# Kernel tuning notes

Measured on AMD Instinct MI355X. Metric: run time of the kernel, lower is better.

Reference implementation:

```python
import jax, jax.numpy as jnp
import numpy as np

HEADS = 4
KS = 7  # neighborhood window size


def group_norm(x, g, b, eps=1e-5):
    # GroupNorm(1, C) on NCHW: normalize over (C,H,W) per sample
    mu = x.mean(axis=(1, 2, 3), keepdims=True)
    var = x.var(axis=(1, 2, 3), keepdims=True)
    xn = (x - mu) * jax.lax.rsqrt(var + eps)
    return xn * g[None, :, None, None] + b[None, :, None, None]


def layer_norm(x, g, b, eps=1e-5):
    mu = x.mean(axis=-1, keepdims=True)
    var = x.var(axis=-1, keepdims=True)
    return (x - mu) * jax.lax.rsqrt(var + eps) * g + b


def na2d(x, qkv_w, qkv_b, proj_w, proj_b, rpb):
    # Neighborhood attention 2D (NATTEN semantics: window clamped at borders)
    N, H, W, C = x.shape
    e, k = HEADS, KS
    d = C // e
    qkv = x @ qkv_w.T + qkv_b  # [N,H,W,3C]
    q, kk, v = jnp.split(qkv, 3, axis=-1)
    q = q.reshape(N, H, W, e, d) * (d ** -0.5)
    kk = kk.reshape(N, H, W, e, d)
    v = v.reshape(N, H, W, e, d)
    ni = jnp.clip(jnp.arange(H) - k // 2, 0, H - k)[:, None] + jnp.arange(k)  # [H,k]
    nj = jnp.clip(jnp.arange(W) - k // 2, 0, W - k)[:, None] + jnp.arange(k)  # [W,k]
    kg = kk[:, ni][:, :, :, nj]  # [N,H,i,W,j,e,d]
    vg = v[:, ni][:, :, :, nj]
    scores = jnp.einsum('nhwed,nhiwjed->nhweij', q, kg)  # [N,H,W,e,k,k]
    ri = ni - jnp.arange(H)[:, None] + (k - 1)  # rel pos index in [0, 2k-2]
    rj = nj - jnp.arange(W)[:, None] + (k - 1)
    bias = rpb[:, ri][:, :, :, rj]  # [e,H,i,W,j]
    scores = scores + bias.transpose(1, 3, 0, 2, 4)[None]
    attn = jax.nn.softmax(scores.reshape(N, H, W, e, k * k), axis=-1).reshape(N, H, W, e, k, k)
    out = jnp.einsum('nhweij,nhiwjed->nhwed', attn, vg).reshape(N, H, W, C)
    return out @ proj_w.T + proj_b


def na_layer(x, gn_g, gn_b, qkv_w, qkv_b, proj_w, proj_b, rpb, ln_g, ln_b, fc1_w, fc1_b, fc2_w, fc2_b):
    N, C, H, W = x.shape
    x1 = x.transpose(0, 2, 3, 1)  # n h w c (pre-norm residual)
    xg = group_norm(x, gn_g, gn_b).transpose(0, 2, 3, 1)
    a = na2d(xg, qkv_w, qkv_b, proj_w, proj_b, rpb) + x1
    t = a.reshape(N, H * W, C)
    h = jax.nn.gelu(layer_norm(t, ln_g, ln_b) @ fc1_w.T + fc1_b, approximate=False)
    t = t + (h @ fc2_w.T + fc2_b)
    return t.reshape(N, H, W, C).transpose(0, 3, 1, 2)


def conv3x3(x, w, b):
    y = jax.lax.conv_general_dilated(x, w, (1, 1), 'SAME', dimension_numbers=('NCHW', 'OIHW', 'NCHW'))
    return y + b[None, :, None, None]


def setup_inputs() -> dict:
    key = jax.random.key(0)
    ks = jax.random.split(key, 16)
    N, C, H, W = 2, 128, 64, 64
    L, e, k, hid, red = 2, HEADS, KS, 4 * 128, 18
    rn = lambda kk, shape, s=0.02: jax.random.normal(kk, shape, jnp.float32) * s
    return {
        'x': jax.random.normal(ks[0], (N, C, H, W), jnp.float32),
        'gn_g': jnp.ones((L, C), jnp.float32), 'gn_b': jnp.zeros((L, C), jnp.float32),
        'qkv_w': rn(ks[1], (L, 3 * C, C)), 'qkv_b': jnp.zeros((L, 3 * C), jnp.float32),
        'proj_w': rn(ks[2], (L, C, C)), 'proj_b': jnp.zeros((L, C), jnp.float32),
        'rpb': rn(ks[3], (L, e, 2 * k - 1, 2 * k - 1)),
        'ln_g': jnp.ones((L, C), jnp.float32), 'ln_b': jnp.zeros((L, C), jnp.float32),
        'fc1_w': rn(ks[4], (L, hid, C)), 'fc1_b': jnp.zeros((L, hid), jnp.float32),
        'fc2_w': rn(ks[5], (L, C, hid)), 'fc2_b': jnp.zeros((L, C), jnp.float32),
        'bconv_w': rn(ks[6], (C, C, 3, 3)), 'bconv_b': jnp.zeros((C,), jnp.float32),
        'c1_w': rn(ks[7], (C // 4, C)), 'c1_b': jnp.zeros((C // 4,), jnp.float32),
        'c2_w': rn(ks[8], (C, C // 4)), 'c2_b': jnp.zeros((C,), jnp.float32),
        'ca1_w': rn(ks[9], (C // red, C)), 'ca1_b': jnp.zeros((C // red,), jnp.float32),
        'ca2_w': rn(ks[10], (C, C // red)), 'ca2_b': jnp.zeros((C,), jnp.float32),
    }


def reference(x, gn_g, gn_b, qkv_w, qkv_b, proj_w, proj_b, rpb, ln_g, ln_b, fc1_w, fc1_b, fc2_w, fc2_b, bconv_w, bconv_b, c1_w, c1_b, c2_w, c2_b, ca1_w, ca1_b, ca2_w, ca2_b):
    res = x
    for l in range(gn_g.shape[0]):  # n_resblocks (structurally fixed, small)
        res = na_layer(res, gn_g[l], gn_b[l], qkv_w[l], qkv_b[l], proj_w[l], proj_b[l], rpb[l],
                       ln_g[l], ln_b[l], fc1_w[l], fc1_b[l], fc2_w[l], fc2_b[l])
    res = conv3x3(res, bconv_w, bconv_b)
    # tail: 1x1 conv -> ReLU -> 1x1 conv -> CALayer
    y = jax.nn.relu(jnp.einsum('rc,nchw->nrhw', c1_w, res) + c1_b[None, :, None, None])
    y = jnp.einsum('cr,nrhw->nchw', c2_w, y) + c2_b[None, :, None, None]
    p = y.mean(axis=(2, 3))  # global avg pool -> [N,C]
    s = jax.nn.sigmoid(jax.nn.relu(p @ ca1_w.T + ca1_b) @ ca2_w.T + ca2_b)
    y = y * s[:, :, None, None]
    return y + x
```

## Files before the change

### kernel.cpp

```cpp
#include <hip/hip_runtime.h>
#include <math.h>

typedef unsigned short u16;

#define NN 2
#define CC 128
#define HH 64
#define WW 64
#define NHD 4
#define DH 32
#define KSZ 7
#define PIX (NN*HH*WW)
#define HID 512
#define C4 32
#define CRED 7
#define RW 22
#define RNB 160
#define NBV 154

typedef float f32x4 __attribute__((ext_vector_type(4)));
typedef short bf16x8 __attribute__((ext_vector_type(8)));

static __device__ __forceinline__ float u2f(u16 u){ return __uint_as_float(((unsigned)u) << 16); }
static __device__ __forceinline__ u16 f2u(float f){
    unsigned b = __float_as_uint(f);
    return (u16)((b + 0x7FFFu + ((b >> 16) & 1u)) >> 16);
}

__global__ void detect_k(const u16* __restrict__ x, int* __restrict__ flag,
                         float* __restrict__ poolacc){
    __shared__ float red[256];
    int t = threadIdx.x;
    float mx = 0.f;
    for(int i = t; i < 4096; i += 256){
        float v = fabsf(u2f(x[i]));
        if(v < 1e30f) mx = fmaxf(mx, v);
    }
    red[t] = mx; __syncthreads();
    for(int s = 128; s > 0; s >>= 1){
        if(t < s) red[t] = fmaxf(red[t], red[t+s]);
        __syncthreads();
    }
    if(t == 0) *flag = (red[0] > 1e6f) ? 1 : 0;
    if(t < NN*CC) poolacc[t] = 0.f;
}

struct PtrTab { const void* p[23]; int off[24]; };
#define NCVT 2172
#define NRPK 576
#define NNCH 512

__global__ __launch_bounds__(256) void setup_k(
    PtrTab tab, u16* __restrict__ Wb, u16* __restrict__ Wt,
    const void* __restrict__ convw, const void* __restrict__ x,
    float* __restrict__ cur, float* __restrict__ part,
    const int* __restrict__ flag, int total)
{
    int blk = blockIdx.x;
    int t = threadIdx.x;
    int fl = *flag;
    if(blk < NCVT){
        int i = blk*256 + t;
        if(i < total){
            int a = 0;
            while(i >= tab.off[a+1]) a++;
            int loc = i - tab.off[a];
            Wb[i] = fl ? f2u(((const float*)tab.p[a])[loc]) : ((const u16*)tab.p[a])[loc];
        }
        return;
    }
    if(blk < NCVT + NRPK){
        int i = (blk - NCVT)*256 + t;
        if(i < CC*CC*9){
            int o = i/(9*CC); int rem = i%(9*CC); int tap = rem/CC; int c = rem%CC;
            size_t s = (size_t)(o*CC + c)*9 + tap;
            Wt[i] = fl ? f2u(((const float*)convw)[s]) : ((const u16*)convw)[s];
        }
        return;
    }
    __shared__ float tile[32][65];
    __shared__ float wred[4][2];
    int u = blk - NCVT - NRPK;
    int bx = u & 3, by = u >> 2;
    int n = by >> 6, i = by & 63;
    for(int idx = t; idx < 32*64; idx += 256){
        int cl = idx >> 6, j = idx & 63;
        size_t src = ((size_t)(n*CC + bx*32 + cl)*HH + i)*WW + j;
        tile[cl][j] = fl ? ((const float*)x)[src] : u2f(((const u16*)x)[src]);
    }
    __syncthreads();
    float s = 0.f, q = 0.f;
    for(int idx = t; idx < 64*32; idx += 256){
        int j = idx >> 5, cl = idx & 31;
        float v = tile[cl][j];
        cur[((size_t)((n*HH + i)*WW) + j)*CC + bx*32 + cl] = v;
        s += v; q += v*v;
    }
    #pragma unroll
    for(int off = 32; off > 0; off >>= 1){ s += __shfl_xor(s, off, 64); q += __shfl_xor(q, off, 64); }
    int wave = t >> 6;
    if((t & 63) == 0){ wred[wave][0] = s; wred[wave][1] = q; }
    __syncthreads();
    if(t == 0){
        float ss = wred[0][0]+wred[1][0]+wred[2][0]+wred[3][0];
        float qq = wred[0][1]+wred[1][1]+wred[2][1]+wred[3][1];
        int pidx = n*256 + i*4 + bx;
        part[pidx*2] = ss; part[pidx*2+1] = qq;
    }
}

enum { EPI_NONE = 0, EPI_RES = 1, EPI_GELU = 2 };
enum { OUT_F32 = 0, OUT_BF16 = 1, OUT_BOTH = 2 };
enum { EX_NONE = 0, EX_STATS = 1 };
#define LDP 136

template<int EPI, int OUTM, int AGN, int EXTRA>
__global__ __launch_bounds__(256) void g64_k(
    const void* __restrict__ Av, const u16* __restrict__ W, const u16* __restrict__ bias,
    const float* __restrict__ R, float* __restrict__ Cf, u16* __restrict__ Cb,
    const u16* __restrict__ gnw, const u16* __restrict__ gnb,
    float* __restrict__ gnpart, int gncount,
    int M, int N, int K)
{
    __shared__ __align__(16) u16 As[64*LDP];
    __shared__ __align__(16) u16 Bs[64*LDP];
    __shared__ float wred[4][2];
    const int bm = blockIdx.y*64, bn = blockIdx.x*64;
    const int t = threadIdx.x;
    const int wave = t >> 6, lane = t & 63;
    const int wm = (wave >> 1)*32, wn = (wave & 1)*32;
    const int lg = lane >> 4, lr = lane & 15;
    const int nsm = bm >> 12;
    f32x4 acc[2][2];
    #pragma unroll
    for(int i = 0; i < 2; i++)
        #pragma unroll
        for(int j = 0; j < 2; j++) acc[i][j] = (f32x4){0.f,0.f,0.f,0.f};

    float gmu = 0.f, grs = 0.f;
    if(AGN){
        float a = 0.f, q = 0.f;
        for(int idx = lane; idx < gncount; idx += 64){
            a += gnpart[(nsm*gncount + idx)*2];
            q += gnpart[(nsm*gncount + idx)*2 + 1];
        }
        #pragma unroll
        for(int off = 32; off > 0; off >>= 1){
            a += __shfl_xor(a, off, 64); q += __shfl_xor(q, off, 64);
        }
        const float inv = 1.f/(float)(HH*WW*CC);
        gmu = a*inv;
        grs = rsqrtf(fmaxf(q*inv - gmu*gmu, 0.f) + 1e-5f);
    }

    for(int k0 = 0; k0 < K; k0 += 128){
        uint4 ra[4], rb[4];
        float4 fa[4][2];
        #pragma unroll
        for(int r = 0; r < 4; r++){
            int e = r*256 + t;
            int row = e >> 4, ch = e & 15;
            if(AGN){
                const float* ap = (const float*)Av + (size_t)(bm+row)*K + k0 + ch*8;
                fa[r][0] = *(const float4*)ap;
                fa[r][1] = *(const float4*)(ap + 4);
            } else {
                ra[r] = *(const uint4*)((const u16*)Av + (size_t)(bm+row)*K + k0 + ch*8);
            }
            rb[r] = (bn+row < N) ? *(const uint4*)(W + (size_t)(bn+row)*K + k0 + ch*8)
                                 : (uint4){0,0,0,0};
        }
        #pragma unroll
        for(int r = 0; r < 4; r++){
            int e = r*256 + t;
            int row = e >> 4, ch = e & 15;
            if(AGN){
                union { uint4 u; u16 h[8]; } g8, b8, o8;
                g8.u = *(const uint4*)(gnw + k0 + ch*8);
                b8.u = *(const uint4*)(gnb + k0 + ch*8);
                const float* fv = (const float*)&fa[r][0];
                #pragma unroll
                for(int z = 0; z < 8; z++)
                    o8.h[z] = f2u((fv[z]-gmu)*grs*u2f(g8.h[z]) + u2f(b8.h[z]));
                *(uint4*)&As[row*LDP + ch*8] = o8.u;
            } else {
                *(uint4*)&As[row*LDP + ch*8] = ra[r];
            }
            *(uint4*)&Bs[row*LDP + ch*8] = rb[r];
        }
        __syncthreads();
        #pragma unroll
        for(int kc = 0; kc < 4; kc++){
            bf16x8 af0 = *(const bf16x8*)&As[(wm + lr)*LDP      + kc*32 + lg*8];
            bf16x8 af1 = *(const bf16x8*)&As[(wm + 16 + lr)*LDP + kc*32 + lg*8];
            bf16x8 bf0 = *(const bf16x8*)&Bs[(wn + lr)*LDP      + kc*32 + lg*8];
            bf16x8 bf1 = *(const bf16x8*)&Bs[(wn + 16 + lr)*LDP + kc*32 + lg*8];
            acc[0][0] = __builtin_amdgcn_mfma_f32_16x16x32_bf16(af0, bf0, acc[0][0], 0, 0, 0);
            acc[0][1] = __builtin_amdgcn_mfma_f32_16x16x32_bf16(af0, bf1, acc[0][1], 0, 0, 0);
            acc[1][0] = __builtin_amdgcn_mfma_f32_16x16x32_bf16(af1, bf0, acc[1][0], 0, 0, 0);
            acc[1][1] = __builtin_amdgcn_mfma_f32_16x16x32_bf16(af1, bf1, acc[1][1], 0, 0, 0);
        }
        if(k0 + 128 < K) __syncthreads();
    }

    float ssum = 0.f, sq = 0.f;
    #pragma unroll
    for(int i = 0; i < 2; i++){
        #pragma unroll
        for(int j = 0; j < 2; j++){
            int col = bn + wn + j*16 + lr;
            if(col >= N) continue;
            #pragma unroll
            for(int reg = 0; reg < 4; reg++){
                int row = bm + wm + i*16 + lg*4 + reg;
                float v = acc[i][j][reg] + u2f(bias[col]);
                if(EPI == EPI_RES)  v += R[(size_t)row*N + col];
                if(EPI == EPI_GELU) v = 0.5f*v*(1.f + erff(v*0.70710678118f));
                if(OUTM == OUT_F32 || OUTM == OUT_BOTH) Cf[(size_t)row*N + col] = v;
                if(OUTM == OUT_BF16 || OUTM == OUT_BOTH) Cb[(size_t)row*N + col] = f2u(v);
                if(EXTRA == EX_STATS){ ssum += v; sq += v*v; }
            }
        }
    }
    if(EXTRA == EX_STATS){
        #pragma unroll
        for(int off = 32; off > 0; off >>= 1){
            ssum += __shfl_xor(ssum, off, 64); sq += __shfl_xor(sq, off, 64);
        }
        if(lane == 0){ wred[wave][0] = ssum; wred[wave][1] = sq; }
        __syncthreads();
        if(t == 0){
            int bidx = blockIdx.y*gridDim.x + blockIdx.x;
            gnpart[bidx*2]   = wred[0][0]+wred[1][0]+wred[2][0]+wred[3][0];
            gnpart[bidx*2+1] = wred[0][1]+wred[1][1]+wred[2][1]+wred[3][1];
        }
    }
}

__global__ __launch_bounds__(256) void proj_ln_k(
    const u16* __restrict__ A, const u16* __restrict__ W, const u16* __restrict__ bias,
    const float* __restrict__ R, const u16* __restrict__ lng, const u16* __restrict__ lnb,
    float* __restrict__ abuf, u16* __restrict__ lnout)
{
    __shared__ __align__(16) u16 As[64*LDP];
    __shared__ __align__(16) u16 Bs[128*LDP];
    __shared__ float redS[64][2], redQ[64][2], muS[64], rsS[64];
    const int bm = blockIdx.x*64;
    const int t = threadIdx.x;
    const int wave = t >> 6, lane = t & 63;
    const int wm = (wave >> 1)*32, wn = (wave & 1)*64;
    const int lg = lane >> 4, lr = lane & 15;

    {
        uint4 ra[4], rb[8];
        #pragma unroll
        for(int r = 0; r < 4; r++){
            int e = r*256 + t; int row = e >> 4, ch = e & 15;
            ra[r] = *(const uint4*)(A + (size_t)(bm+row)*CC + ch*8);
        }
        #pragma unroll
        for(int r = 0; r < 8; r++){
            int e = r*256 + t; int row = e >> 4, ch = e & 15;
            rb[r] = *(const uint4*)(W + (size_t)row*CC + ch*8);
        }
        #pragma unroll
        for(int r = 0; r < 4; r++){
            int e = r*256 + t; int row = e >> 4, ch = e & 15;
            *(uint4*)&As[row*LDP + ch*8] = ra[r];
        }
        #pragma unroll
        for(int r = 0; r < 8; r++){
            int e = r*256 + t; int row = e >> 4, ch = e & 15;
            *(uint4*)&Bs[row*LDP + ch*8] = rb[r];
        }
    }
    __syncthreads();

    f32x4 acc[2][4];
    #pragma unroll
    for(int i = 0; i < 2; i++)
        #pragma unroll
        for(int j = 0; j < 4; j++) acc[i][j] = (f32x4){0.f,0.f,0.f,0.f};
    #pragma unroll
    for(int kc = 0; kc < 4; kc++){
        bf16x8 af[2], bf[4];
        #pragma unroll
        for(int i = 0; i < 2; i++)
            af[i] = *(const bf16x8*)&As[(wm + i*16 + lr)*LDP + kc*32 + lg*8];
        #pragma unroll
        for(int j = 0; j < 4; j++)
            bf[j] = *(const bf16x8*)&Bs[(wn + j*16 + lr)*LDP + kc*32 + lg*8];
        #pragma unroll
        for(int i = 0; i < 2; i++)
            #pragma unroll
            for(int j = 0; j < 4; j++)
                acc[i][j] = __builtin_amdgcn_mfma_f32_16x16x32_bf16(af[i], bf[j], acc[i][j], 0, 0, 0);
    }
    #pragma unroll
    for(int i = 0; i < 2; i++){
        #pragma unroll
        for(int reg = 0; reg < 4; reg++){
            int rl = wm + i*16 + lg*4 + reg;
            float rs_ = 0.f, rq_ = 0.f;
            #pragma unroll
            for(int j = 0; j < 4; j++){
                int col = wn + j*16 + lr;
                float v = acc[i][j][reg] + u2f(bias[col]) + R[(size_t)(bm+rl)*CC + col];
                acc[i][j][reg] = v;
                abuf[(size_t)(bm+rl)*CC + col] = v;
                rs_ += v; rq_ += v*v;
            }
            rs_ += __shfl_xor(rs_, 1, 64); rq_ += __shfl_xor(rq_, 1, 64);
            rs_ += __shfl_xor(rs_, 2, 64); rq_ += __shfl_xor(rq_, 2, 64);
            rs_ += __shfl_xor(rs_, 4, 64); rq_ += __shfl_xor(rq_, 4, 64);
            rs_ += __shfl_xor(rs_, 8, 64); rq_ += __shfl_xor(rq_, 8, 64);
            if(lr == 0){ redS[rl][wn>>6] = rs_; redQ[rl][wn>>6] = rq_; }
        }
    }
    __syncthreads();
    if(t < 64){
        float mu = (redS[t][0] + redS[t][1])*(1.f/CC);
        float var = fmaxf((redQ[t][0] + redQ[t][1])*(1.f/CC) - mu*mu, 0.f);
        muS[t] = mu; rsS[t] = rsqrtf(var + 1e-5f);
    }
    __syncthreads();
    #pragma unroll
    for(int i = 0; i < 2; i++){
        #pragma unroll
        for(int reg = 0; reg < 4; reg++){
            int rl = wm + i*16 + lg*4 + reg;
            float mu = muS[rl], rstd = rsS[rl];
            #pragma unroll
            for(int j = 0; j < 4; j++){
                int col = wn + j*16 + lr;
                float v = (acc[i][j][reg] - mu)*rstd*u2f(lng[col]) + u2f(lnb[col]);
                lnout[(size_t)(bm+rl)*CC + col] = f2u(v);
            }
        }
    }
}

__global__ __launch_bounds__(256) void mconv_k(
    const u16* __restrict__ in, const u16* __restrict__ Wt,
    const u16* __restrict__ bias, u16* __restrict__ Cb)
{
    __shared__ __align__(16) u16 As[64*LDP];
    __shared__ __align__(16) u16 Bs[64*LDP];
    const int bm = blockIdx.y*64, bn = blockIdx.x*64;
    const int t = threadIdx.x;
    const int wave = t >> 6, lane = t & 63;
    const int wm = (wave >> 1)*32, wn = (wave & 1)*32;
    const int lg = lane >> 4, lr = lane & 15;
    f32x4 acc[2][2];
    #pragma unroll
    for(int i = 0; i < 2; i++)
        #pragma unroll
        for(int j = 0; j < 2; j++) acc[i][j] = (f32x4){0.f,0.f,0.f,0.f};

    for(int tap = 0; tap < 9; tap++){
        int dy = tap/3 - 1, dx = tap%3 - 1;
        int k0 = tap*128;
        uint4 ra[4], rb[4];
        #pragma unroll
        for(int r = 0; r < 4; r++){
            int e = r*256 + t;
            int row = e >> 4, ch = e & 15;
            int p = bm + row;
            int n = p >> 12, ii = (p & 4095) >> 6, jj = p & 63;
            int y = ii + dy, x = jj + dx;
            ra[r] = (uint4){0,0,0,0};
            if(y >= 0 && y < HH && x >= 0 && x < WW)
                ra[r] = *(const uint4*)(in + (size_t)(((n*HH + y)*WW + x))*CC + ch*8);
            rb[r] = *(const uint4*)(Wt + (size_t)(bn+row)*(9*CC) + k0 + ch*8);
        }
        #pragma unroll
        for(int r = 0; r < 4; r++){
            int e = r*256 + t;
            int row = e >> 4, ch = e & 15;
            *(uint4*)&As[row*LDP + ch*8] = ra[r];
            *(uint4*)&Bs[row*LDP + ch*8] = rb[r];
        }
        __syncthreads();
        #pragma unroll
        for(int kc = 0; kc < 4; kc++){
            bf16x8 af0 = *(const bf16x8*)&As[(wm + lr)*LDP      + kc*32 + lg*8];
            bf16x8 af1 = *(const bf16x8*)&As[(wm + 16 + lr)*LDP + kc*32 + lg*8];
            bf16x8 bf0 = *(const bf16x8*)&Bs[(wn + lr)*LDP      + kc*32 + lg*8];
            bf16x8 bf1 = *(const bf16x8*)&Bs[(wn + 16 + lr)*LDP + kc*32 + lg*8];
            acc[0][0] = __builtin_amdgcn_mfma_f32_16x16x32_bf16(af0, bf0, acc[0][0], 0, 0, 0);
            acc[0][1] = __builtin_amdgcn_mfma_f32_16x16x32_bf16(af0, bf1, acc[0][1], 0, 0, 0);
            acc[1][0] = __builtin_amdgcn_mfma_f32_16x16x32_bf16(af1, bf0, acc[1][0], 0, 0, 0);
            acc[1][1] = __builtin_amdgcn_mfma_f32_16x16x32_bf16(af1, bf1, acc[1][1], 0, 0, 0);
        }
        if(tap < 8) __syncthreads();
    }
    #pragma unroll
    for(int i = 0; i < 2; i++){
        #pragma unroll
        for(int j = 0; j < 2; j++){
            int col = bn + wn + j*16 + lr;
            #pragma unroll
            for(int reg = 0; reg < 4; reg++){
                int row = bm + wm + i*16 + lg*4 + reg;
                Cb[(size_t)row*CC + col] = f2u(acc[i][j][reg] + u2f(bias[col]));
            }
        }
    }
}

#define KVP 72
#define PSP 168

__global__ __launch_bounds__(128) void att_tile_k(
    const u16* __restrict__ qkv, const u16* __restrict__ rpb, u16* __restrict__ out)
{
    __shared__ __align__(16) u16 KV[2][RNB][KVP];
    __shared__ __align__(16) u16 Qs[16][64];
    __shared__ __align__(16) u16 Ps[2][16][PSP];
    __shared__ float rpbs[2][169];
    const int blk = blockIdx.x;
    const int rb = blk >> 1, eg = blk & 1;
    const int p0 = rb*16;
    const int jb = p0 & 63, i = (p0 >> 6) & 63, n = p0 >> 12;
    const int i0 = min(max(i-3, 0), HH-KSZ);
    const int rc0 = min(max(jb-3, 0), WW-KSZ);
    const int t = threadIdx.x;

    for(int idx = t; idx < 2*169; idx += 128)
        rpbs[idx/169][idx%169] = u2f(rpb[(eg*2 + idx/169)*169 + idx%169]);
    {
        int pix = t >> 3, ch = t & 7;
        *(uint4*)&Qs[pix][ch*8] = *(const uint4*)(qkv + (size_t)(p0+pix)*(3*CC) + eg*64 + ch*8);
    }
    for(int idx = t; idx < RNB*16; idx += 128){
        int nb = idx >> 4, part = idx & 15;
        int kv = part >> 3, ch = part & 7;
        uint4 v = (uint4){0,0,0,0};
        if(nb < NBV){
            int ky = nb/RW, kcol = nb - ky*RW;
            int sy = i0 + ky, sx = min(rc0 + kcol, WW-1);
            v = *(const uint4*)(qkv + (size_t)((n*HH + sy)*WW + sx)*(3*CC) + CC + kv*CC + eg*64 + ch*8);
        }
        *(uint4*)&KV[kv][nb][ch*8] = v;
    }
    __syncthreads();

    const int el = t >> 6;
    const int lane = t & 63, lg = lane >> 4, lr = lane & 15;

    bf16x8 aq = *(const bf16x8*)&Qs[lr][el*32 + lg*8];
    f32x4 sc[10];
    #pragma unroll
    for(int c = 0; c < 10; c++){
        bf16x8 bk = *(const bf16x8*)&KV[0][c*16+lr][el*32 + lg*8];
        sc[c] = __builtin_amdgcn_mfma_f32_16x16x32_bf16(aq, bk, (f32x4){0.f,0.f,0.f,0.f}, 0, 0, 0);
    }
    #pragma unroll
    for(int reg = 0; reg < 4; reg++){
        int pix = lg*4 + reg;
        int j = jb + pix;
        int base = min(max(j-3, 0), WW-KSZ) - rc0;
        float mx = -1e30f;
        #pragma unroll
        for(int c = 0; c < 10; c++){
            int nb = c*16 + lr;
            int ky = nb/RW, kcol = nb - ky*RW;
            float v = -1e30f;
            if(nb < NBV && kcol >= base && kcol <= base+6){
                int ri = i0 + ky - i + (KSZ-1);
                int rj = rc0 + kcol - j + (KSZ-1);
                v = sc[c][reg]*0.17677669529663689f + rpbs[el][ri*13 + rj];
            }
            sc[c][reg] = v;
            mx = fmaxf(mx, v);
        }
        mx = fmaxf(mx, __shfl_xor(mx, 1, 64));
        mx = fmaxf(mx, __shfl_xor(mx, 2, 64));
        mx = fmaxf(mx, __shfl_xor(mx, 4, 64));
        mx = fmaxf(mx, __shfl_xor(mx, 8, 64));
        float sum = 0.f;
        #pragma unroll
        for(int c = 0; c < 10; c++){
            float p = __expf(sc[c][reg] - mx);
            sc[c][reg] = p; sum += p;
        }
        sum += __shfl_xor(sum, 1, 64);
        sum += __shfl_xor(sum, 2, 64);
        sum += __shfl_xor(sum, 4, 64);
        sum += __shfl_xor(sum, 8, 64);
        float rs = 1.f/sum;
        #pragma unroll
        for(int c = 0; c < 10; c++)
            Ps[el][pix][c*16+lr] = f2u(sc[c][reg]*rs);
    }
    __syncthreads();
    f32x4 o0 = (f32x4){0.f,0.f,0.f,0.f}, o1 = (f32x4){0.f,0.f,0.f,0.f};
    #pragma unroll
    for(int ks = 0; ks < 5; ks++){
        bf16x8 ap = *(const bf16x8*)&Ps[el][lr][ks*32 + lg*8];
        bf16x8 b0, b1;
        #pragma unroll
        for(int jj = 0; jj < 8; jj++){
            int nb = ks*32 + lg*8 + jj;
            b0[jj] = (short)KV[1][nb][el*32 + lr];
            b1[jj] = (short)KV[1][nb][el*32 + 16 + lr];
        }
        o0 = __builtin_amdgcn_mfma_f32_16x16x32_bf16(ap, b0, o0, 0, 0, 0);
        o1 = __builtin_amdgcn_mfma_f32_16x16x32_bf16(ap, b1, o1, 0, 0, 0);
    }
    int e = eg*2 + el;
    #pragma unroll
    for(int reg = 0; reg < 4; reg++){
        int pix = lg*4 + reg;
        out[(size_t)(p0+pix)*CC + e*32 + lr]      = f2u(o0[reg]);
        out[(size_t)(p0+pix)*CC + e*32 + 16 + lr] = f2u(o1[reg]);
    }
}

__global__ __launch_bounds__(256) void tail_k(
    const u16* __restrict__ A, const u16* __restrict__ c1w, const u16* __restrict__ c1b,
    const u16* __restrict__ c2w, const u16* __restrict__ c2b,
    float* __restrict__ ybuf, float* __restrict__ poolacc)
{
    __shared__ __align__(16) u16 As[64*LDP];
    __shared__ __align__(16) u16 Bs1[32*LDP];
    __shared__ __align__(16) u16 Hs[64*40];
    __shared__ __align__(16) u16 Bs2[128*40];
    const int bm = blockIdx.x*64;
    const int t = threadIdx.x;
    const int wave = t >> 6, lane = t & 63;
    const int lg = lane >> 4, lr = lane & 15;
    const int nsm = bm >> 12;

    {
        uint4 ra[4], rb1[2], rb2[2];
        #pragma unroll
        for(int r = 0; r < 4; r++){
            int e = r*256 + t; int row = e >> 4, ch = e & 15;
            ra[r] = *(const uint4*)(A + (size_t)(bm+row)*CC + ch*8);
        }
        #pragma unroll
        for(int r = 0; r < 2; r++){
            int e = r*256 + t; int row = e >> 4, ch = e & 15;
            rb1[r] = *(const uint4*)(c1w + (size_t)row*CC + ch*8);
        }
        #pragma unroll
        for(int r = 0; r < 2; r++){
            int e = r*256 + t; int row = e >> 2, ch = e & 3;
            rb2[r] = *(const uint4*)(c2w + (size_t)row*C4 + ch*8);
        }
        #pragma unroll
        for(int r = 0; r < 4; r++){
            int e = r*256 + t; int row = e >> 4, ch = e & 15;
            *(uint4*)&As[row*LDP + ch*8] = ra[r];
        }
        #pragma unroll
        for(int r = 0; r < 2; r++){
            int e = r*256 + t; int row = e >> 4, ch = e & 15;
            *(uint4*)&Bs1[row*LDP + ch*8] = rb1[r];
        }
        #pragma unroll
        for(int r = 0; r < 2; r++){
            int e = r*256 + t; int row = e >> 2, ch = e & 3;
            *(uint4*)&Bs2[row*40 + ch*8] = rb2[r];
        }
    }
    __syncthreads();

    {
        const int wm1 = (wave >> 1)*32, wn1 = (wave & 1)*16;
        f32x4 a1[2];
        a1[0] = (f32x4){0.f,0.f,0.f,0.f}; a1[1] = (f32x4){0.f,0.f,0.f,0.f};
        #pragma unroll
        for(int kc = 0; kc < 4; kc++){
            bf16x8 bf = *(const bf16x8*)&Bs1[(wn1 + lr)*LDP + kc*32 + lg*8];
            bf16x8 af0 = *(const bf16x8*)&As[(wm1 + lr)*LDP      + kc*32 + lg*8];
            bf16x8 af1 = *(const bf16x8*)&As[(wm1 + 16 + lr)*LDP + kc*32 + lg*8];
            a1[0] = __builtin_amdgcn_mfma_f32_16x16x32_bf16(af0, bf, a1[0], 0, 0, 0);
            a1[1] = __builtin_amdgcn_mfma_f32_16x16x32_bf16(af1, bf, a1[1], 0, 0, 0);
        }
        #pragma unroll
        for(int i = 0; i < 2; i++){
            #pragma unroll
            for(int reg = 0; reg < 4; reg++){
                int rl = wm1 + i*16 + lg*4 + reg;
                int col = wn1 + lr;
                Hs[rl*40 + col] = f2u(fmaxf(a1[i][reg] + u2f(c1b[col]), 0.f));
            }
        }
    }
    __syncthreads();

    {
        const int wm = (wave >> 1)*32, wn = (wave & 1)*64;
        f32x4 a2[2][4];
        #pragma unroll
        for(int i = 0; i < 2; i++)
            #pragma unroll
            for(int j = 0; j < 4; j++) a2[i][j] = (f32x4){0.f,0.f,0.f,0.f};
        bf16x8 af[2];
        #pragma unroll
        for(int i = 0; i < 2; i++)
            af[i] = *(const bf16x8*)&Hs[(wm + i*16 + lr)*40 + lg*8];
        #pragma unroll
        for(int j = 0; j < 4; j++){
            bf16x8 bf = *(const bf16x8*)&Bs2[(wn + j*16 + lr)*40 + lg*8];
            a2[0][j] = __builtin_amdgcn_mfma_f32_16x16x32_bf16(af[0], bf, a2[0][j], 0, 0, 0);
            a2[1][j] = __builtin_amdgcn_mfma_f32_16x16x32_bf16(af[1], bf, a2[1][j], 0, 0, 0);
        }
        float cs[4] = {0.f,0.f,0.f,0.f};
        #pragma unroll
        for(int i = 0; i < 2; i++){
            #pragma unroll
            for(int j = 0; j < 4; j++){
                int col = wn + j*16 + lr;
                #pragma unroll
                for(int reg = 0; reg < 4; reg++){
                    int row = bm + wm + i*16 + lg*4 + reg;
                    float v = a2[i][j][reg] + u2f(c2b[col]);
                    ybuf[(size_t)row*CC + col] = v;
                    cs[j] += v;
                }
            }
        }
        #pragma unroll
        for(int j = 0; j < 4; j++){
            cs[j] += __shfl_xor(cs[j], 16, 64);
            cs[j] += __shfl_xor(cs[j], 32, 64);
        }
        if(lg == 0){
            #pragma unroll
            for(int j = 0; j < 4; j++)
                atomicAdd(&poolacc[nsm*CC + wn + j*16 + lr], cs[j]);
        }
    }
}

__global__ __launch_bounds__(256) void final_ca_k(
    const float* __restrict__ y, const float* __restrict__ poolacc,
    const u16* __restrict__ w1, const u16* __restrict__ b1,
    const u16* __restrict__ w2, const u16* __restrict__ b2,
    const void* __restrict__ xraw, void* __restrict__ outv,
    const int* __restrict__ flag)
{
    __shared__ float t1s[CRED];
    __shared__ float sres;
    int id0 = blockIdx.x*256;
    int c = (id0 >> 12) & (CC-1);
    int n = id0 >> 19;
    int t = threadIdx.x;
    if(t < CRED){
        float a = u2f(b1[t]);
        const float pscale = 1.f/(float)(HH*WW);
        for(int cc = 0; cc < CC; cc++)
            a += poolacc[n*CC + cc]*pscale*u2f(w1[t*CC + cc]);
        t1s[t] = fmaxf(a, 0.f);
    }
    __syncthreads();
    if(t == 0){
        float a = u2f(b2[c]);
        #pragma unroll
        for(int r = 0; r < CRED; r++) a += t1s[r]*u2f(w2[c*CRED + r]);
        sres = 1.f/(1.f + __expf(-a));
    }
    __syncthreads();
    float s = sres;
    int id = id0 + t;
    int j = id & 63; int i = (id >> 6) & 63;
    float xr = (*flag) ? ((const float*)xraw)[id] : u2f(((const u16*)xraw)[id]);
    float v = y[(size_t)((n*HH + i)*WW + j)*CC + c]*s + xr;
    if(*flag) ((float*)outv)[id] = v;
    else      ((u16*)outv)[id] = f2u(v);
}

extern "C" void kernel_launch(void* const* d_in, const int* in_sizes, int n_in,
                              void* d_out, int out_size, void* d_ws, size_t ws_size,
                              hipStream_t stream){
    float* wsf    = (float*)d_ws;
    int*   flagp  = (int*)d_ws;
    float* gnpart = wsf + 8;
    float* poolacc= wsf + 1040;

    u16* Wb = (u16*)(wsf + 2048);
    static const int wsizes[23] = {256,256,98304,768,32768,256,1352,256,256,131072,1024,
                                   131072,256,147456,128,4096,32,4096,128,896,7,896,128};
    int woff[24]; woff[0] = 0;
    for(int i = 0; i < 23; i++) woff[i+1] = woff[i] + wsizes[i];
    const int WTOT = woff[23];
    u16* Wt = Wb + 555760;

    float* AB    = wsf + 360448;
    float* cur   = AB;
    u16*  cur16  = (u16*)(AB + 1048576);
    u16*  xg16   = (u16*)(AB + 1572864);
    u16*  qkv16  = (u16*)(AB + 2097152);
    float* abuf  = AB + 2097152;
    u16*  hbuf16 = (u16*)(AB + 3670016);
    float* ybuf  = AB + 3670016;

    detect_k<<<1, 256, 0, stream>>>((const u16*)d_in[0], flagp, poolacc);

    PtrTab tab;
    for(int i = 0; i < 23; i++){ tab.p[i] = d_in[i+1]; tab.off[i] = woff[i]; }
    tab.off[23] = woff[23];
    setup_k<<<NCVT + NRPK + NNCH, 256, 0, stream>>>(
        tab, Wb, Wt, d_in[14], d_in[0], cur, gnpart, flagp, WTOT);

    const u16 *gng = Wb+woff[0], *gnb = Wb+woff[1], *qkvw = Wb+woff[2], *qkvb = Wb+woff[3],
              *projw = Wb+woff[4], *projb = Wb+woff[5], *rpbw = Wb+woff[6], *lng = Wb+woff[7],
              *lnb = Wb+woff[8], *f1w = Wb+woff[9], *f1b = Wb+woff[10], *f2w = Wb+woff[11],
              *f2b = Wb+woff[12], *bcb = Wb+woff[14], *c1w = Wb+woff[15],
              *c1b = Wb+woff[16], *c2w = Wb+woff[17], *c2b = Wb+woff[18], *ca1w = Wb+woff[19],
              *ca1b = Wb+woff[20], *ca2w = Wb+woff[21], *ca2b = Wb+woff[22];

    for(int l = 0; l < 2; l++){
        int gncount = (l == 0) ? 256 : 128;

        g64_k<EPI_NONE,OUT_BF16,1,EX_NONE><<<dim3(6, PIX/64), 256, 0, stream>>>(
            cur, qkvw + (size_t)l*3*CC*CC, qkvb + l*3*CC, nullptr, nullptr, qkv16,
            gng + l*CC, gnb + l*CC, gnpart, gncount, PIX, 3*CC, CC);

        att_tile_k<<<PIX/16*2, 128, 0, stream>>>(qkv16, rpbw + l*NHD*169, xg16);

        proj_ln_k<<<PIX/64, 256, 0, stream>>>(
            xg16, projw + (size_t)l*CC*CC, projb + l*CC, cur, lng + l*CC, lnb + l*CC,
            abuf, xg16);

        g64_k<EPI_GELU,OUT_BF16,0,EX_NONE><<<dim3(8, PIX/64), 256, 0, stream>>>(
            xg16, f1w + (size_t)l*HID*CC, f1b + l*HID, nullptr, nullptr, hbuf16,
            nullptr, nullptr, nullptr, 0, PIX, HID, CC);

        g64_k<EPI_RES,OUT_BOTH,0,EX_STATS><<<dim3(2, PIX/64), 256, 0, stream>>>(
            hbuf16, f2w + (size_t)l*CC*HID, f2b + l*CC, abuf, cur, cur16,
            nullptr, nullptr, gnpart, 0, PIX, CC, HID);
    }

    mconv_k<<<dim3(2, PIX/64), 256, 0, stream>>>(cur16, Wt, bcb, xg16);

    tail_k<<<PIX/64, 256, 0, stream>>>(xg16, c1w, c1b, c2w, c2b, ybuf, poolacc);

    final_ca_k<<<(NN*CC*HH*WW)/256, 256, 0, stream>>>(
        ybuf, poolacc, ca1w, ca1b, ca2w, ca2b, d_in[0], d_out, flagp);
}
```

Measured before the change: 268.9 us.

## Prefetch next K tile in GEMM and conv, fold detect into setup kernel

Register-prefetches the next K-tile (or conv tap) while MFMAs run on the current tile in the GEMM and 3x3 conv kernels, so global loads overlap with compute. K becomes a template constant, which allows full unrolling. The separate detect launch is folded into setup_k, with every block recomputing the input-format flag itself. The attention kernel reuses the KV shared buffer for the probabilities, cutting LDS use but adding a barrier. Prefetching raises register pressure, and the redundant flag scan adds work to every setup block.

```diff
diff --git a/kernel.cpp b/kernel.cpp
--- a/kernel.cpp
+++ b/kernel.cpp
@@ -27,24 +27,6 @@
     return (u16)((b + 0x7FFFu + ((b >> 16) & 1u)) >> 16);
 }
 
-__global__ void detect_k(const u16* __restrict__ x, int* __restrict__ flag,
-                         float* __restrict__ poolacc){
-    __shared__ float red[256];
-    int t = threadIdx.x;
-    float mx = 0.f;
-    for(int i = t; i < 4096; i += 256){
-        float v = fabsf(u2f(x[i]));
-        if(v < 1e30f) mx = fmaxf(mx, v);
-    }
-    red[t] = mx; __syncthreads();
-    for(int s = 128; s > 0; s >>= 1){
-        if(t < s) red[t] = fmaxf(red[t], red[t+s]);
-        __syncthreads();
-    }
-    if(t == 0) *flag = (red[0] > 1e6f) ? 1 : 0;
-    if(t < NN*CC) poolacc[t] = 0.f;
-}
-
 struct PtrTab { const void* p[23]; int off[24]; };
 #define NCVT 2172
 #define NRPK 576
@@ -54,11 +36,29 @@
     PtrTab tab, u16* __restrict__ Wb, u16* __restrict__ Wt,
     const void* __restrict__ convw, const void* __restrict__ x,
     float* __restrict__ cur, float* __restrict__ part,
-    const int* __restrict__ flag, int total)
+    int* __restrict__ flagp, float* __restrict__ poolacc, int total)
 {
-    int blk = blockIdx.x;
-    int t = threadIdx.x;
-    int fl = *flag;
+    __shared__ float red[4];
+    __shared__ float tile[32][65];
+    __shared__ float wred[4][2];
+    const int blk = blockIdx.x, t = threadIdx.x;
+
+    const u16* xr = (const u16*)x;
+    float mx = 0.f;
+    for(int i = t; i < 4096; i += 256){
+        float v = fabsf(u2f(xr[i]));
+        if(v < 1e30f) mx = fmaxf(mx, v);
+    }
+    #pragma unroll
+    for(int off = 32; off > 0; off >>= 1) mx = fmaxf(mx, __shfl_xor(mx, off, 64));
+    if((t & 63) == 0) red[t >> 6] = mx;
+    __syncthreads();
+    const int fl = (fmaxf(fmaxf(red[0], red[1]), fmaxf(red[2], red[3])) > 1e6f) ? 1 : 0;
+    if(blk == 0){
+        if(t == 0) *flagp = fl;
+        if(t < NN*CC) poolacc[t] = 0.f;
+    }
+
     if(blk < NCVT){
         int i = blk*256 + t;
         if(i < total){
@@ -78,8 +78,6 @@
         }
         return;
     }
-    __shared__ float tile[32][65];
-    __shared__ float wred[4][2];
     int u = blk - NCVT - NRPK;
     int bx = u & 3, by = u >> 2;
     int n = by >> 6, i = by & 63;
@@ -114,14 +112,15 @@
 enum { EX_NONE = 0, EX_STATS = 1 };
 #define LDP 136
 
-template<int EPI, int OUTM, int AGN, int EXTRA>
+template<int KTILES, int EPI, int OUTM, int AGN, int EXTRA>
 __global__ __launch_bounds__(256) void g64_k(
     const void* __restrict__ Av, const u16* __restrict__ W, const u16* __restrict__ bias,
     const float* __restrict__ R, float* __restrict__ Cf, u16* __restrict__ Cb,
     const u16* __restrict__ gnw, const u16* __restrict__ gnb,
     float* __restrict__ gnpart, int gncount,
-    int M, int N, int K)
+    int M, int N)
 {
+    const int K = KTILES*128;
     __shared__ __align__(16) u16 As[64*LDP];
     __shared__ __align__(16) u16 Bs[64*LDP];
     __shared__ float wred[4][2];
@@ -153,31 +152,37 @@
         grs = rsqrtf(fmaxf(q*inv - gmu*gmu, 0.f) + 1e-5f);
     }
 
-    for(int k0 = 0; k0 < K; k0 += 128){
-        uint4 ra[4], rb[4];
-        float4 fa[4][2];
+    auto load_tile = [&](int kt, uint4* ra, float4 (*fa)[2], uint4* rb){
         #pragma unroll
         for(int r = 0; r < 4; r++){
             int e = r*256 + t;
             int row = e >> 4, ch = e & 15;
             if(AGN){
-                const float* ap = (const float*)Av + (size_t)(bm+row)*K + k0 + ch*8;
+                const float* ap = (const float*)Av + (size_t)(bm+row)*K + kt*128 + ch*8;
                 fa[r][0] = *(const float4*)ap;
                 fa[r][1] = *(const float4*)(ap + 4);
             } else {
-                ra[r] = *(const uint4*)((const u16*)Av + (size_t)(bm+row)*K + k0 + ch*8);
-            }
-            rb[r] = (bn+row < N) ? *(const uint4*)(W + (size_t)(bn+row)*K + k0 + ch*8)
+                ra[r] = *(const uint4*)((const u16*)Av + (size_t)(bm+row)*K + kt*128 + ch*8);
+            }
+            rb[r] = (bn+row < N) ? *(const uint4*)(W + (size_t)(bn+row)*K + kt*128 + ch*8)
                                  : (uint4){0,0,0,0};
         }
+    };
+
+    uint4 ra[4], rb[4];
+    float4 fa[4][2];
+    load_tile(0, ra, fa, rb);
+
+    #pragma unroll
+    for(int kt = 0; kt < KTILES; kt++){
         #pragma unroll
         for(int r = 0; r < 4; r++){
             int e = r*256 + t;
             int row = e >> 4, ch = e & 15;
             if(AGN){
                 union { uint4 u; u16 h[8]; } g8, b8, o8;
-                g8.u = *(const uint4*)(gnw + k0 + ch*8);
-                b8.u = *(const uint4*)(gnb + k0 + ch*8);
+                g8.u = *(const uint4*)(gnw + kt*128 + ch*8);
+                b8.u = *(const uint4*)(gnb + kt*128 + ch*8);
                 const float* fv = (const float*)&fa[r][0];
                 #pragma unroll
                 for(int z = 0; z < 8; z++)
@@ -189,6 +194,8 @@
             *(uint4*)&Bs[row*LDP + ch*8] = rb[r];
         }
         __syncthreads();
+        uint4 pa[4], pb[4]; float4 pf[4][2];
+        if(kt + 1 < KTILES) load_tile(kt + 1, pa, pf, pb);
         #pragma unroll
         for(int kc = 0; kc < 4; kc++){
             bf16x8 af0 = *(const bf16x8*)&As[(wm + lr)*LDP      + kc*32 + lg*8];
@@ -200,7 +207,11 @@
             acc[1][0] = __builtin_amdgcn_mfma_f32_16x16x32_bf16(af1, bf0, acc[1][0], 0, 0, 0);
             acc[1][1] = __builtin_amdgcn_mfma_f32_16x16x32_bf16(af1, bf1, acc[1][1], 0, 0, 0);
         }
-        if(k0 + 128 < K) __syncthreads();
+        if(kt + 1 < KTILES){
+            __syncthreads();
+            #pragma unroll
+            for(int r = 0; r < 4; r++){ ra[r] = pa[r]; rb[r] = pb[r]; fa[r][0] = pf[r][0]; fa[r][1] = pf[r][1]; }
+        }
     }
 
     float ssum = 0.f, sq = 0.f;
@@ -357,10 +368,8 @@
         #pragma unroll
         for(int j = 0; j < 2; j++) acc[i][j] = (f32x4){0.f,0.f,0.f,0.f};
 
-    for(int tap = 0; tap < 9; tap++){
+    auto load_tap = [&](int tap, uint4* ra, uint4* rb){
         int dy = tap/3 - 1, dx = tap%3 - 1;
-        int k0 = tap*128;
-        uint4 ra[4], rb[4];
         #pragma unroll
         for(int r = 0; r < 4; r++){
             int e = r*256 + t;
@@ -371,8 +380,14 @@
             ra[r] = (uint4){0,0,0,0};
             if(y >= 0 && y < HH && x >= 0 && x < WW)
                 ra[r] = *(const uint4*)(in + (size_t)(((n*HH + y)*WW + x))*CC + ch*8);
-            rb[r] = *(const uint4*)(Wt + (size_t)(bn+row)*(9*CC) + k0 + ch*8);
-        }
+            rb[r] = *(const uint4*)(Wt + (size_t)(bn+row)*(9*CC) + tap*128 + ch*8);
+        }
+    };
+
+    uint4 ra[4], rb[4];
+    load_tap(0, ra, rb);
+    #pragma unroll
+    for(int tap = 0; tap < 9; tap++){
         #pragma unroll
         for(int r = 0; r < 4; r++){
             int e = r*256 + t;
@@ -381,6 +396,8 @@
             *(uint4*)&Bs[row*LDP + ch*8] = rb[r];
         }
         __syncthreads();
+        uint4 pa[4], pb[4];
+        if(tap < 8) load_tap(tap + 1, pa, pb);
         #pragma unroll
         for(int kc = 0; kc < 4; kc++){
             bf16x8 af0 = *(const bf16x8*)&As[(wm + lr)*LDP      + kc*32 + lg*8];
@@ -392,7 +409,11 @@
             acc[1][0] = __builtin_amdgcn_mfma_f32_16x16x32_bf16(af1, bf0, acc[1][0], 0, 0, 0);
             acc[1][1] = __builtin_amdgcn_mfma_f32_16x16x32_bf16(af1, bf1, acc[1][1], 0, 0, 0);
         }
-        if(tap < 8) __syncthreads();
+        if(tap < 8){
+            __syncthreads();
+            #pragma unroll
+            for(int r = 0; r < 4; r++){ ra[r] = pa[r]; rb[r] = pb[r]; }
+        }
     }
     #pragma unroll
     for(int i = 0; i < 2; i++){
@@ -416,8 +437,8 @@
 {
     __shared__ __align__(16) u16 KV[2][RNB][KVP];
     __shared__ __align__(16) u16 Qs[16][64];
-    __shared__ __align__(16) u16 Ps[2][16][PSP];
     __shared__ float rpbs[2][169];
+    u16* PsB = &KV[0][0][0];
     const int blk = blockIdx.x;
     const int rb = blk >> 1, eg = blk & 1;
     const int p0 = rb*16;
@@ -455,6 +476,7 @@
         bf16x8 bk = *(const bf16x8*)&KV[0][c*16+lr][el*32 + lg*8];
         sc[c] = __builtin_amdgcn_mfma_f32_16x16x32_bf16(aq, bk, (f32x4){0.f,0.f,0.f,0.f}, 0, 0, 0);
     }
+    __syncthreads();
     #pragma unroll
     for(int reg = 0; reg < 4; reg++){
         int pix = lg*4 + reg;
@@ -491,13 +513,13 @@
         float rs = 1.f/sum;
         #pragma unroll
         for(int c = 0; c < 10; c++)
-            Ps[el][pix][c*16+lr] = f2u(sc[c][reg]*rs);
+            PsB[(el*16 + pix)*PSP + c*16 + lr] = f2u(sc[c][reg]*rs);
     }
     __syncthreads();
     f32x4 o0 = (f32x4){0.f,0.f,0.f,0.f}, o1 = (f32x4){0.f,0.f,0.f,0.f};
     #pragma unroll
     for(int ks = 0; ks < 5; ks++){
-        bf16x8 ap = *(const bf16x8*)&Ps[el][lr][ks*32 + lg*8];
+        bf16x8 ap = *(const bf16x8*)&PsB[(el*16 + lr)*PSP + ks*32 + lg*8];
         bf16x8 b0, b1;
         #pragma unroll
         for(int jj = 0; jj < 8; jj++){
@@ -698,13 +720,11 @@
     u16*  hbuf16 = (u16*)(AB + 3670016);
     float* ybuf  = AB + 3670016;
 
-    detect_k<<<1, 256, 0, stream>>>((const u16*)d_in[0], flagp, poolacc);
-
     PtrTab tab;
     for(int i = 0; i < 23; i++){ tab.p[i] = d_in[i+1]; tab.off[i] = woff[i]; }
     tab.off[23] = woff[23];
     setup_k<<<NCVT + NRPK + NNCH, 256, 0, stream>>>(
-        tab, Wb, Wt, d_in[14], d_in[0], cur, gnpart, flagp, WTOT);
+        tab, Wb, Wt, d_in[14], d_in[0], cur, gnpart, flagp, poolacc, WTOT);
 
     const u16 *gng = Wb+woff[0], *gnb = Wb+woff[1], *qkvw = Wb+woff[2], *qkvb = Wb+woff[3],
               *projw = Wb+woff[4], *projb = Wb+woff[5], *rpbw = Wb+woff[6], *lng = Wb+woff[7],
@@ -716,9 +736,9 @@
     for(int l = 0; l < 2; l++){
         int gncount = (l == 0) ? 256 : 128;
 
-        g64_k<EPI_NONE,OUT_BF16,1,EX_NONE><<<dim3(6, PIX/64), 256, 0, stream>>>(
+        g64_k<1,EPI_NONE,OUT_BF16,1,EX_NONE><<<dim3(6, PIX/64), 256, 0, stream>>>(
             cur, qkvw + (size_t)l*3*CC*CC, qkvb + l*3*CC, nullptr, nullptr, qkv16,
-            gng + l*CC, gnb + l*CC, gnpart, gncount, PIX, 3*CC, CC);
+            gng + l*CC, gnb + l*CC, gnpart, gncount, PIX, 3*CC);
 
         att_tile_k<<<PIX/16*2, 128, 0, stream>>>(qkv16, rpbw + l*NHD*169, xg16);
 
@@ -726,13 +746,13 @@
             xg16, projw + (size_t)l*CC*CC, projb + l*CC, cur, lng + l*CC, lnb + l*CC,
             abuf, xg16);
 
-        g64_k<EPI_GELU,OUT_BF16,0,EX_NONE><<<dim3(8, PIX/64), 256, 0, stream>>>(
+        g64_k<1,EPI_GELU,OUT_BF16,0,EX_NONE><<<dim3(8, PIX/64), 256, 0, stream>>>(
             xg16, f1w + (size_t)l*HID*CC, f1b + l*HID, nullptr, nullptr, hbuf16,
-            nullptr, nullptr, nullptr, 0, PIX, HID, CC);
-
-        g64_k<EPI_RES,OUT_BOTH,0,EX_STATS><<<dim3(2, PIX/64), 256, 0, stream>>>(
+            nullptr, nullptr, nullptr, 0, PIX, HID);
+
+        g64_k<4,EPI_RES,OUT_BOTH,0,EX_STATS><<<dim3(2, PIX/64), 256, 0, stream>>>(
             hbuf16, f2w + (size_t)l*CC*HID, f2b + l*CC, abuf, cur, cur16,
-            nullptr, nullptr, gnpart, 0, PIX, CC, HID);
+            nullptr, nullptr, gnpart, 0, PIX, CC);
     }
 
     mconv_k<<<dim3(2, PIX/64), 256, 0, stream>>>(cur16, Wt, bcb, xg16);
```

Result: slower. 309.7 us (+15.2%).
